# Kernel tuning notes

Measured on AMD Instinct MI355X. Metric: run time of the kernel, lower is better.

## Reference

```python
import jax, jax.numpy as jnp
import numpy as np

# static graph/layer sizes
N_SRC0, N_DST0 = 60000, 15000
N_DST1 = 4000
H1, D1 = 8, 256   # layer1: 8 heads, 256 per head
H2, D2 = 1, 128   # layer2: 1 head, 128 (= out_feats)
IN_DIM = H1 * D1  # 2048


def gat_conv(feat, W, al, ar, b, src, dst, n_dst, H, D, act):
    # feat: [N_src, F]; W: [F, H*D]; al/ar: [H, D]; b: [H*D]
    h = (feat @ W).reshape(feat.shape[0], H, D)          # [N_src, H, D]
    el = jnp.einsum('nhd,hd->nh', h, al)                 # [N_src, H]
    er = jnp.einsum('nhd,hd->nh', h[:n_dst], ar)         # [N_dst, H]
    e = jax.nn.leaky_relu(el[src] + er[dst], 0.2)        # [E, H]
    # edge softmax grouped by destination node (numerically stable)
    emax = jax.ops.segment_max(e, dst, num_segments=n_dst)
    emax = jnp.where(jnp.isfinite(emax), emax, 0.0)      # guard zero-in-degree dsts
    ex = jnp.exp(e - emax[dst])
    denom = jax.ops.segment_sum(ex, dst, num_segments=n_dst)
    a = ex / denom[dst]                                  # [E, H]
    out = jax.ops.segment_sum(h[src] * a[:, :, None], dst, num_segments=n_dst)
    out = out + b.reshape(1, H, D)
    return jax.nn.relu(out) if act else out              # [N_dst, H, D]


def setup_inputs() -> dict:
    key = jax.random.key(0)
    ks = jax.random.split(key, 16)
    feat = jax.random.normal(ks[0], (N_SRC0, IN_DIM), dtype=jnp.float32)
    src0 = jax.random.randint(ks[1], (240000,), 0, N_SRC0, dtype=jnp.int32)
    dst0 = jax.random.randint(ks[2], (240000,), 0, N_DST0, dtype=jnp.int32)
    src1 = jax.random.randint(ks[3], (64000,), 0, N_DST0, dtype=jnp.int32)
    dst1 = jax.random.randint(ks[4], (64000,), 0, N_DST1, dtype=jnp.int32)
    # layer1 params (in 2048 -> 8 heads x 256)
    W1 = jax.random.normal(ks[5], (IN_DIM, H1 * D1), dtype=jnp.float32) / np.sqrt(IN_DIM)
    al1 = jax.random.normal(ks[6], (H1, D1), dtype=jnp.float32) / np.sqrt(D1)
    ar1 = jax.random.normal(ks[7], (H1, D1), dtype=jnp.float32) / np.sqrt(D1)
    b1 = jnp.zeros((H1 * D1,), dtype=jnp.float32)
    # layer2 params (in 256 (post head-mean) -> 1 head x 128)
    W2 = jax.random.normal(ks[8], (D1, H2 * D2), dtype=jnp.float32) / np.sqrt(D1)
    al2 = jax.random.normal(ks[9], (H2, D2), dtype=jnp.float32) / np.sqrt(D2)
    ar2 = jax.random.normal(ks[10], (H2, D2), dtype=jnp.float32) / np.sqrt(D2)
    b2 = jnp.zeros((H2 * D2,), dtype=jnp.float32)
    return {"feat": feat, "W1": W1, "al1": al1, "ar1": ar1, "b1": b1,
            "W2": W2, "al2": al2, "ar2": ar2, "b2": b2,
            "src0": src0, "dst0": dst0, "src1": src1, "dst1": dst1}


def reference(feat, W1, al1, ar1, b1, W2, al2, ar2, b2, src0, dst0, src1, dst1):
    h = gat_conv(feat, W1, al1, ar1, b1, src0, dst0, N_DST0, H1, D1, act=True)
    h = h.mean(axis=1)                                   # head mean -> [N_DST0, 256]
    h = gat_conv(h, W2, al2, ar2, b2, src1, dst1, N_DST1, H2, D2, act=False)
    return h.reshape(N_DST1, H2 * D2)                    # flatten(1) -> [4000, 128]
```

## Files before the change

kernel.cpp:

```cpp
#include <hip/hip_runtime.h>
#include <hip/hip_bf16.h>


typedef __bf16 bf16;
typedef bf16 bf16x8 __attribute__((ext_vector_type(8)));
typedef float f32x4 __attribute__((ext_vector_type(4)));

#define N_SRC0V 60000
#define N_DST0V 15000
#define N_DST1V 4000
#define E0V 240000
#define E1V 64000
#define HD1V 2048
#define K1V 2048
#define M1PAD 60032
#define M2PAD 15104

#define BM 128
#define BN 128
#define BK 64

__device__ __forceinline__ void gload16(const void* g, void* l) {
  __builtin_amdgcn_global_load_lds(
      (__attribute__((address_space(1))) void*)(g),
      (__attribute__((address_space(3))) void*)(l), 16, 0, 0);
}

__global__ void k_convert(const float* __restrict__ x, bf16* __restrict__ y, long n8) {
  long i = (long)blockIdx.x * 256 + threadIdx.x;
  if (i >= n8) return;
  const float4* xp = (const float4*)(x + i * 8);
  float4 a = xp[0], b = xp[1];
  bf16x8 o;
  o[0] = (bf16)a.x; o[1] = (bf16)a.y; o[2] = (bf16)a.z; o[3] = (bf16)a.w;
  o[4] = (bf16)b.x; o[5] = (bf16)b.y; o[6] = (bf16)b.z; o[7] = (bf16)b.w;
  *(bf16x8*)(y + i * 8) = o;
}

__global__ void k_transpose_bf16(const float* __restrict__ W, bf16* __restrict__ WT,
                                 int R, int C) {
  __shared__ float tile[32][33];
  int tx = threadIdx.x & 31, ty = threadIdx.x >> 5;
  int c0 = blockIdx.x * 32, r0 = blockIdx.y * 32;
  for (int i = ty; i < 32; i += 8) {
    int r = r0 + i, c = c0 + tx;
    tile[i][tx] = (r < R && c < C) ? W[(size_t)r * C + c] : 0.f;
  }
  __syncthreads();
  for (int i = ty; i < 32; i += 8) {
    int c = c0 + i, r = r0 + tx;
    if (c < C && r < R) WT[(size_t)c * R + r] = (bf16)tile[tx][i];
  }
}

template <typename OutT>
__global__ __launch_bounds__(256) void k_gemm_bt(
    const bf16* __restrict__ A, const bf16* __restrict__ BT,
    OutT* __restrict__ C, int N, int K) {
  __shared__ bf16 sA[BM * BK];
  __shared__ bf16 sB[BN * BK];
  const int tid = threadIdx.x;
  const int lane = tid & 63;
  const int wv = tid >> 6;
  const int wm = wv >> 1, wn = wv & 1;
  const int lr = lane & 15, lq = lane >> 4;
  const int m0 = blockIdx.y * BM;
  const int n0 = blockIdx.x * BN;

  const f32x4 vzero = {0.f, 0.f, 0.f, 0.f};
  f32x4 acc[4][4];
#pragma unroll
  for (int i = 0; i < 4; ++i)
#pragma unroll
    for (int j = 0; j < 4; ++j) acc[i][j] = vzero;

  for (int k0 = 0; k0 < K; k0 += BK) {
#pragma unroll
    for (int it = 0; it < 4; ++it) {
      int c = it * 256 + tid;
      int seg = c >> 6;
      int ln = c & 63;
      int row = (seg >> 1) * 16 + (ln & 15);
      int col = (seg & 1) * 32 + (ln >> 4) * 8;
      gload16(A + (size_t)(m0 + row) * K + k0 + col, &sA[c * 8]);
      gload16(BT + (size_t)(n0 + row) * K + k0 + col, &sB[c * 8]);
    }
    __syncthreads();
#pragma unroll
    for (int kk = 0; kk < BK; kk += 32) {
      const int kb = kk >> 5;
      bf16x8 af[4], bfr[4];
#pragma unroll
      for (int i = 0; i < 4; ++i)
        af[i] = *(const bf16x8*)&sA[(((wm * 4 + i) * 2 + kb) * 64 + lane) * 8];
#pragma unroll
      for (int j = 0; j < 4; ++j)
        bfr[j] = *(const bf16x8*)&sB[(((wn * 4 + j) * 2 + kb) * 64 + lane) * 8];
#pragma unroll
      for (int i = 0; i < 4; ++i)
#pragma unroll
        for (int j = 0; j < 4; ++j)
          acc[i][j] = __builtin_amdgcn_mfma_f32_16x16x32_bf16(af[i], bfr[j], acc[i][j], 0, 0, 0);
    }
    __syncthreads();
  }
#pragma unroll
  for (int i = 0; i < 4; ++i)
#pragma unroll
    for (int j = 0; j < 4; ++j) {
      int row = m0 + wm * 64 + i * 16 + lq * 4;
      int col = n0 + wn * 64 + j * 16 + lr;
#pragma unroll
      for (int r = 0; r < 4; ++r)
        C[(size_t)(row + r) * N + col] = (OutT)acc[i][j][r];
    }
}

__global__ void k_el_er1(const bf16* __restrict__ h, const float* __restrict__ al,
                         const float* __restrict__ ar, float* __restrict__ el,
                         float* __restrict__ er, int n_dst) {
  int row = blockIdx.x;
  int t = threadIdx.x;
  bf16x8 hv = *(const bf16x8*)(h + (size_t)row * 2048 + t * 8);
  float pl = 0.f, pr = 0.f;
#pragma unroll
  for (int e = 0; e < 8; ++e) {
    float v = (float)hv[e];
    pl += v * al[t * 8 + e];
    pr += v * ar[t * 8 + e];
  }
#pragma unroll
  for (int off = 16; off >= 1; off >>= 1) {
    pl += __shfl_down(pl, off);
    pr += __shfl_down(pr, off);
  }
  if ((t & 31) == 0) {
    el[(size_t)row * 8 + (t >> 5)] = pl;
    if (row < n_dst) er[(size_t)row * 8 + (t >> 5)] = pr;
  }
}

__global__ void k_el_er2(const float* __restrict__ h, const float* __restrict__ al,
                         const float* __restrict__ ar, float* __restrict__ el,
                         float* __restrict__ er, int n_el, int n_dst) {
  int t = threadIdx.x;
  int row = blockIdx.x * 16 + (t >> 4);
  int s = t & 15;
  const float* hp = h + (size_t)row * 128 + s * 8;
  float4 a = *(const float4*)hp;
  float4 b = *(const float4*)(hp + 4);
  float pl = a.x * al[s * 8] + a.y * al[s * 8 + 1] + a.z * al[s * 8 + 2] + a.w * al[s * 8 + 3]
           + b.x * al[s * 8 + 4] + b.y * al[s * 8 + 5] + b.z * al[s * 8 + 6] + b.w * al[s * 8 + 7];
  float pr = a.x * ar[s * 8] + a.y * ar[s * 8 + 1] + a.z * ar[s * 8 + 2] + a.w * ar[s * 8 + 3]
           + b.x * ar[s * 8 + 4] + b.y * ar[s * 8 + 5] + b.z * ar[s * 8 + 6] + b.w * ar[s * 8 + 7];
#pragma unroll
  for (int off = 8; off >= 1; off >>= 1) {
    pl += __shfl_down(pl, off);
    pr += __shfl_down(pr, off);
  }
  if (s == 0 && row < n_el) {
    el[row] = pl;
    if (row < n_dst) er[row] = pr;
  }
}

__global__ void k_zero(int* __restrict__ p, int n) {
  int i = blockIdx.x * 256 + threadIdx.x;
  if (i < n) p[i] = 0;
}
__global__ void k_hist(const int* __restrict__ d, int E, int* __restrict__ counts) {
  int e = blockIdx.x * 256 + threadIdx.x;
  if (e < E) atomicAdd(&counts[d[e]], 1);
}
__global__ void k_scan(const int* __restrict__ counts, int n, int* __restrict__ offs,
                       int* __restrict__ cursor) {
  __shared__ int part[1024];
  int t = threadIdx.x;
  int per = (n + 1023) >> 10;
  int b = t * per;
  int e = b + per < n ? b + per : n;
  int s = 0;
  for (int i = b; i < e; ++i) s += counts[i];
  part[t] = s;
  __syncthreads();
  for (int off = 1; off < 1024; off <<= 1) {
    int v = 0;
    if (t >= off) v = part[t - off];
    __syncthreads();
    part[t] += v;
    __syncthreads();
  }
  int run = (t == 0) ? 0 : part[t - 1];
  for (int i = b; i < e; ++i) { offs[i] = run; cursor[i] = run; run += counts[i]; }
  if (t == 1023) offs[n] = run;
}
__global__ void k_scatter(const int* __restrict__ d, int E, int* __restrict__ cursor,
                          int* __restrict__ eperm) {
  int e = blockIdx.x * 256 + threadIdx.x;
  if (e < E) eperm[atomicAdd(&cursor[d[e]], 1)] = e;
}

__global__ void k_stats(const int* __restrict__ offs, const int* __restrict__ eperm,
                        const int* __restrict__ srcv, const float* __restrict__ el,
                        const float* __restrict__ er, int n_dst, int H,
                        float* __restrict__ emax, float* __restrict__ eden) {
  int idx = blockIdx.x * 256 + threadIdx.x;
  if (idx >= n_dst * H) return;
  int dn = idx / H, hh = idx - dn * H;
  int s0 = offs[dn], s1 = offs[dn + 1];
  float erv = er[idx];
  float mx = -1e30f;
  for (int p = s0; p < s1; ++p) {
    float v = el[srcv[eperm[p]] * H + hh] + erv;
    v = v > 0.f ? v : 0.2f * v;
    mx = fmaxf(mx, v);
  }
  if (s1 == s0) mx = 0.f;
  float s = 0.f;
  for (int p = s0; p < s1; ++p) {
    float v = el[srcv[eperm[p]] * H + hh] + erv;
    v = v > 0.f ? v : 0.2f * v;
    s += expf(v - mx);
  }
  emax[idx] = mx;
  eden[idx] = s;
}

__global__ __launch_bounds__(256) void k_aggr1(
    const int* __restrict__ offs, const int* __restrict__ eperm,
    const int* __restrict__ srcv, const float* __restrict__ el,
    const float* __restrict__ er, const float* __restrict__ emax,
    const float* __restrict__ eden, const bf16* __restrict__ h1,
    const float* __restrict__ b1, bf16* __restrict__ outm) {
  int dn = blockIdx.x;
  int t = threadIdx.x;
  int head = t >> 5;
  int jd = (t & 31) << 3;
  __shared__ float wbuf[32][8];
  __shared__ int sidx[32];
  __shared__ float obuf[2048];
  float acc[8] = {0.f, 0.f, 0.f, 0.f, 0.f, 0.f, 0.f, 0.f};
  int s0 = offs[dn], s1 = offs[dn + 1];
  for (int base = s0; base < s1; base += 32) {
    int rem = s1 - base;
    int cnt = rem < 32 ? rem : 32;
    __syncthreads();
    if (t < cnt * 8) {
      int ec = t >> 3, hh = t & 7;
      int e = eperm[base + ec];
      int sv = srcv[e];
      if (hh == 0) sidx[ec] = sv;
      float v = el[sv * 8 + hh] + er[dn * 8 + hh];
      v = v > 0.f ? v : 0.2f * v;
      float den = eden[dn * 8 + hh];
      wbuf[ec][hh] = den > 0.f ? expf(v - emax[dn * 8 + hh]) / den : 0.f;
    }
    __syncthreads();
    for (int ec = 0; ec < cnt; ++ec) {
      float w = wbuf[ec][head];
      const bf16* hp = h1 + (size_t)sidx[ec] * 2048 + (head << 8) + jd;
      bf16x8 x = *(const bf16x8*)hp;
#pragma unroll
      for (int e2 = 0; e2 < 8; ++e2) acc[e2] += w * (float)x[e2];
    }
  }
  int ob = (head << 8) + jd;
#pragma unroll
  for (int k2 = 0; k2 < 8; ++k2) {
    float v = acc[k2] + b1[ob + k2];
    obuf[ob + k2] = v > 0.f ? v : 0.f;
  }
  __syncthreads();
  float sum = 0.f;
#pragma unroll
  for (int hh = 0; hh < 8; ++hh) sum += obuf[hh * 256 + t];
  outm[(size_t)dn * 256 + t] = (bf16)(sum * 0.125f);
}

__global__ __launch_bounds__(128) void k_aggr2(
    const int* __restrict__ offs, const int* __restrict__ eperm,
    const int* __restrict__ srcv, const float* __restrict__ el,
    const float* __restrict__ er, const float* __restrict__ emax,
    const float* __restrict__ eden, const float* __restrict__ h2,
    const float* __restrict__ b2, float* __restrict__ out) {
  int dn = blockIdx.x;
  int t = threadIdx.x;
  __shared__ float wbuf[64];
  __shared__ int sidx[64];
  float acc = 0.f;
  int s0 = offs[dn], s1 = offs[dn + 1];
  float erv = er[dn], mx = emax[dn], den = eden[dn];
  for (int base = s0; base < s1; base += 64) {
    int rem = s1 - base;
    int cnt = rem < 64 ? rem : 64;
    __syncthreads();
    if (t < cnt) {
      int e = eperm[base + t];
      int sv = srcv[e];
      sidx[t] = sv;
      float v = el[sv] + erv;
      v = v > 0.f ? v : 0.2f * v;
      wbuf[t] = den > 0.f ? expf(v - mx) / den : 0.f;
    }
    __syncthreads();
    for (int ec = 0; ec < cnt; ++ec)
      acc += wbuf[ec] * h2[(size_t)sidx[ec] * 128 + t];
  }
  out[(size_t)dn * 128 + t] = acc + b2[t];
}

extern "C" void kernel_launch(void* const* d_in, const int* in_sizes, int n_in,
                              void* d_out, int out_size, void* d_ws, size_t ws_size,
                              hipStream_t stream) {
  const float* feat = (const float*)d_in[0];
  const float* W1   = (const float*)d_in[1];
  const float* al1  = (const float*)d_in[2];
  const float* ar1  = (const float*)d_in[3];
  const float* b1   = (const float*)d_in[4];
  const float* W2   = (const float*)d_in[5];
  const float* al2  = (const float*)d_in[6];
  const float* ar2  = (const float*)d_in[7];
  const float* b2   = (const float*)d_in[8];
  const int* src0   = (const int*)d_in[9];
  const int* dst0   = (const int*)d_in[10];
  const int* src1   = (const int*)d_in[11];
  const int* dst1   = (const int*)d_in[12];
  float* out = (float*)d_out;

  char* w = (char*)d_ws;
  auto alloc = [&](size_t bytes) {
    char* p = w;
    w += (bytes + 255) & ~(size_t)255;
    return p;
  };
  bf16*  featb   = (bf16*)alloc((size_t)M1PAD * K1V * 2);
  bf16*  w1t     = (bf16*)alloc((size_t)HD1V * K1V * 2);
  bf16*  w2t     = (bf16*)alloc((size_t)128 * 256 * 2);
  bf16*  h1      = (bf16*)alloc((size_t)M1PAD * HD1V * 2);
  float* el1     = (float*)alloc((size_t)N_SRC0V * 8 * 4);
  float* er1     = (float*)alloc((size_t)N_DST0V * 8 * 4);
  float* emax1   = (float*)alloc((size_t)N_DST0V * 8 * 4);
  float* eden1   = (float*)alloc((size_t)N_DST0V * 8 * 4);
  bf16*  outm    = (bf16*)alloc((size_t)M2PAD * 256 * 2);
  float* h2      = (float*)alloc((size_t)M2PAD * 128 * 4);
  float* el2     = (float*)alloc((size_t)N_DST0V * 4);
  float* er2     = (float*)alloc((size_t)N_DST1V * 4);
  float* emax2   = (float*)alloc((size_t)N_DST1V * 4);
  float* eden2   = (float*)alloc((size_t)N_DST1V * 4);
  int*   counts1 = (int*)alloc((size_t)N_DST0V * 4);
  int*   offs1   = (int*)alloc((size_t)(N_DST0V + 1) * 4);
  int*   cursor1 = (int*)alloc((size_t)N_DST0V * 4);
  int*   eperm1  = (int*)alloc((size_t)E0V * 4);
  int*   counts2 = (int*)alloc((size_t)N_DST1V * 4);
  int*   offs2   = (int*)alloc((size_t)(N_DST1V + 1) * 4);
  int*   cursor2 = (int*)alloc((size_t)N_DST1V * 4);
  int*   eperm2  = (int*)alloc((size_t)E1V * 4);

  k_zero<<<(N_DST0V + 255) / 256, 256, 0, stream>>>(counts1, N_DST0V);
  k_zero<<<(N_DST1V + 255) / 256, 256, 0, stream>>>(counts2, N_DST1V);
  {
    long n8 = (long)N_SRC0V * K1V / 8;
    k_convert<<<(unsigned)((n8 + 255) / 256), 256, 0, stream>>>(feat, featb, n8);
  }
  k_transpose_bf16<<<dim3(64, 64), 256, 0, stream>>>(W1, w1t, K1V, HD1V);
  k_transpose_bf16<<<dim3(4, 8), 256, 0, stream>>>(W2, w2t, 256, 128);

  k_gemm_bt<bf16><<<dim3(HD1V / BN, M1PAD / BM), 256, 0, stream>>>(featb, w1t, h1, HD1V, K1V);
  k_el_er1<<<N_SRC0V, 256, 0, stream>>>(h1, al1, ar1, el1, er1, N_DST0V);
  k_hist<<<(E0V + 255) / 256, 256, 0, stream>>>(dst0, E0V, counts1);
  k_scan<<<1, 1024, 0, stream>>>(counts1, N_DST0V, offs1, cursor1);
  k_scatter<<<(E0V + 255) / 256, 256, 0, stream>>>(dst0, E0V, cursor1, eperm1);
  k_stats<<<(N_DST0V * 8 + 255) / 256, 256, 0, stream>>>(offs1, eperm1, src0, el1, er1,
                                                         N_DST0V, 8, emax1, eden1);
  k_aggr1<<<N_DST0V, 256, 0, stream>>>(offs1, eperm1, src0, el1, er1, emax1, eden1,
                                       h1, b1, outm);

  k_gemm_bt<float><<<dim3(1, M2PAD / BM), 256, 0, stream>>>(outm, w2t, h2, 128, 256);
  k_el_er2<<<M2PAD / 16, 256, 0, stream>>>(h2, al2, ar2, el2, er2, N_DST0V, N_DST1V);
  k_hist<<<(E1V + 255) / 256, 256, 0, stream>>>(dst1, E1V, counts2);
  k_scan<<<1, 1024, 0, stream>>>(counts2, N_DST1V, offs2, cursor2);
  k_scatter<<<(E1V + 255) / 256, 256, 0, stream>>>(dst1, E1V, cursor2, eperm2);
  k_stats<<<(N_DST1V + 255) / 256, 256, 0, stream>>>(offs2, eperm2, src1, el2, er2,
                                                     N_DST1V, 1, emax2, eden2);
  k_aggr2<<<N_DST1V, 128, 0, stream>>>(offs2, eperm2, src1, el2, er2, emax2, eden2,
                                       h2, b2, out);
}
```

Baseline: 1.995 ms.

## Use 256x256 double-buffered MFMA GEMM with XCD-aware block remap for layer1

Replaces the layer-1 projection GEMM with a new 256x256x64 tiled kernel using 512 threads, double-buffered LDS staging through direct global-to-LDS loads, a fragment-friendly LDS layout, and MFMA priority hints. Workgroup IDs are remapped across the 8 XCDs to improve L2 locality. The M padding grows to a multiple of 256, and the padded rows are zeroed. The larger tile raises reuse per byte loaded, at the cost of 128KB dynamic LDS, high register pressure and lower occupancy.

```diff
diff --git a/kernel.cpp b/kernel.cpp
--- a/kernel.cpp
+++ b/kernel.cpp
@@ -13,12 +13,16 @@
 #define E1V 64000
 #define HD1V 2048
 #define K1V 2048
-#define M1PAD 60032
+#define M1PAD 60160
 #define M2PAD 15104
 
 #define BM 128
 #define BN 128
 #define BK 64
+
+#define GBM 256
+#define GBN 256
+#define GBK 64
 
 __device__ __forceinline__ void gload16(const void* g, void* l) {
   __builtin_amdgcn_global_load_lds(
@@ -51,6 +55,90 @@
     int c = c0 + i, r = r0 + tx;
     if (c < C && r < R) WT[(size_t)c * R + r] = (bf16)tile[tx][i];
   }
+}
+
+__global__ __launch_bounds__(512, 2) void k_gemm256_bt(
+    const bf16* __restrict__ A, const bf16* __restrict__ BT,
+    bf16* __restrict__ C, int N, int K) {
+  extern __shared__ char smem_raw[];
+  bf16* smem = (bf16*)smem_raw;
+  const int tid = threadIdx.x;
+  const int lane = tid & 63;
+  const int wv = tid >> 6;
+  const int wm = wv >> 2;
+  const int wn = wv & 3;
+  const int lr = lane & 15, lq = lane >> 4;
+
+  int nwg = gridDim.x * gridDim.y;
+  int flat = blockIdx.y * gridDim.x + blockIdx.x;
+  if ((nwg & 7) == 0) {
+    int cpx = nwg >> 3;
+    flat = (flat & 7) * cpx + (flat >> 3);
+  }
+  const int m0 = (flat / gridDim.x) * GBM;
+  const int n0 = (flat % gridDim.x) * GBN;
+
+  const f32x4 vzero = {0.f, 0.f, 0.f, 0.f};
+  f32x4 acc[8][4];
+#pragma unroll
+  for (int i = 0; i < 8; ++i)
+#pragma unroll
+    for (int j = 0; j < 4; ++j) acc[i][j] = vzero;
+
+  auto stage = [&](int b, int k0) {
+    bf16* sAb = smem + b * 32768;
+    bf16* sBb = sAb + 16384;
+#pragma unroll
+    for (int it = 0; it < 4; ++it) {
+      int c = it * 512 + tid;
+      int seg = c >> 6;
+      int ln = c & 63;
+      int row = (seg >> 1) * 16 + (ln & 15);
+      int col = (seg & 1) * 32 + (ln >> 4) * 8;
+      gload16(A + (size_t)(m0 + row) * K + k0 + col, &sAb[c * 8]);
+      gload16(BT + (size_t)(n0 + row) * K + k0 + col, &sBb[c * 8]);
+    }
+  };
+
+  const int NT = K / GBK;
+  stage(0, 0);
+  __syncthreads();
+
+  for (int kt = 0; kt < NT; ++kt) {
+    const int cur = kt & 1;
+    bf16* sAb = smem + cur * 32768;
+    bf16* sBb = sAb + 16384;
+    if (kt + 1 < NT) stage(cur ^ 1, (kt + 1) * GBK);
+#pragma unroll
+    for (int kb = 0; kb < 2; ++kb) {
+      bf16x8 af[8], bfr[4];
+#pragma unroll
+      for (int i = 0; i < 8; ++i)
+        af[i] = *(const bf16x8*)&sAb[(((wm * 8 + i) * 2 + kb) * 64 + lane) * 8];
+#pragma unroll
+      for (int j = 0; j < 4; ++j)
+        bfr[j] = *(const bf16x8*)&sBb[(((wn * 4 + j) * 2 + kb) * 64 + lane) * 8];
+      __builtin_amdgcn_s_setprio(1);
+#pragma unroll
+      for (int i = 0; i < 8; ++i)
+#pragma unroll
+        for (int j = 0; j < 4; ++j)
+          acc[i][j] = __builtin_amdgcn_mfma_f32_16x16x32_bf16(af[i], bfr[j], acc[i][j], 0, 0, 0);
+      __builtin_amdgcn_s_setprio(0);
+    }
+    __syncthreads();
+  }
+
+#pragma unroll
+  for (int i = 0; i < 8; ++i)
+#pragma unroll
+    for (int j = 0; j < 4; ++j) {
+      int row = m0 + wm * 128 + i * 16 + lq * 4;
+      int col = n0 + wn * 64 + j * 16 + lr;
+#pragma unroll
+      for (int r = 0; r < 4; ++r)
+        C[(size_t)(row + r) * N + col] = (bf16)acc[i][j][r];
+    }
 }
 
 template <typename OutT>
@@ -326,6 +414,13 @@
   const int* src1   = (const int*)d_in[11];
   const int* dst1   = (const int*)d_in[12];
   float* out = (float*)d_out;
+
+  static bool s_attr_set = false;
+  if (!s_attr_set) {
+    hipFuncSetAttribute(reinterpret_cast<const void*>(k_gemm256_bt),
+                        hipFuncAttributeMaxDynamicSharedMemorySize, 131072);
+    s_attr_set = true;
+  }
 
   char* w = (char*)d_ws;
   auto alloc = [&](size_t bytes) {
@@ -361,11 +456,15 @@
   {
     long n8 = (long)N_SRC0V * K1V / 8;
     k_convert<<<(unsigned)((n8 + 255) / 256), 256, 0, stream>>>(feat, featb, n8);
+    int padi = (M1PAD - N_SRC0V) * K1V / 2;
+    k_zero<<<(padi + 255) / 256, 256, 0, stream>>>(
+        (int*)(featb + (size_t)N_SRC0V * K1V), padi);
   }
   k_transpose_bf16<<<dim3(64, 64), 256, 0, stream>>>(W1, w1t, K1V, HD1V);
   k_transpose_bf16<<<dim3(4, 8), 256, 0, stream>>>(W2, w2t, 256, 128);
 
-  k_gemm_bt<bf16><<<dim3(HD1V / BN, M1PAD / BM), 256, 0, stream>>>(featb, w1t, h1, HD1V, K1V);
+  k_gemm256_bt<<<dim3(HD1V / GBN, M1PAD / GBM), 512, 131072, stream>>>(
+      featb, w1t, h1, HD1V, K1V);
   k_el_er1<<<N_SRC0V, 256, 0, stream>>>(h1, al1, ar1, el1, er1, N_DST0V);
   k_hist<<<(E0V + 255) / 256, 256, 0, stream>>>(dst0, E0V, counts1);
   k_scan<<<1, 1024, 0, stream>>>(counts1, N_DST0V, offs1, cursor1);
```

After: 1.694 ms. 1.18x faster.
